# Performance work log

Measured on AMD Instinct MI355X. Metric: run time of the kernel, lower is better.

Reference implementation:

```python
import jax, jax.numpy as jnp
import numpy as np

B, C, H, W = 4, 256, 64, 64
R, KH, KW = 4, 3, 3
K = KH * KW  # 9 kernel taps


def _conv2d(x, w, b):
    # plain 3x3 conv, stride 1, pad 1, NCHW
    y = jax.lax.conv_general_dilated(x, w, (1, 1), ((1, 1), (1, 1)),
                                     dimension_numbers=('NCHW', 'OIHW', 'NCHW'))
    return y + b[None, :, None, None]


def _bilinear_sample(x, py, px):
    # x: [B,C,H,W]; py,px: [B,K,H,W] float coords; zero padding outside the image.
    B_, C_, H_, W_ = x.shape
    xf = x.reshape(B_, C_, H_ * W_)
    y0 = jnp.floor(py)
    x0 = jnp.floor(px)
    wy = py - y0
    wx = px - x0
    y0i = y0.astype(jnp.int32)
    x0i = x0.astype(jnp.int32)

    def corner(yi, xi, wgt):
        valid = (yi >= 0) & (yi < H_) & (xi >= 0) & (xi < W_)
        idx = (jnp.clip(yi, 0, H_ - 1) * W_ + jnp.clip(xi, 0, W_ - 1)).reshape(B_, -1)
        vals = jax.vmap(lambda xb, ib: jnp.take(xb, ib, axis=1))(xf, idx)  # [B,C,K*H*W]
        vals = vals.reshape(B_, C_, K, H_, W_)
        w_ = (wgt * valid).astype(x.dtype)[:, None]  # [B,1,K,H,W]
        return vals * w_

    out = corner(y0i, x0i, (1 - wy) * (1 - wx))
    out = out + corner(y0i, x0i + 1, (1 - wy) * wx)
    out = out + corner(y0i + 1, x0i, wy * (1 - wx))
    out = out + corner(y0i + 1, x0i + 1, wy * wx)
    return out  # [B,C,K,H,W]


def _deform_conv(x, offset, weight):
    # DCNv1: offset [B, 2K, H, W], interleaved (dy, dx) per kernel tap.
    B_, C_, H_, W_ = x.shape
    off = offset.reshape(B_, K, 2, H_, W_)
    ky, kx = jnp.meshgrid(jnp.arange(KH), jnp.arange(KW), indexing='ij')
    base_y = (ky.reshape(K) - (KH - 1) // 2).astype(x.dtype)
    base_x = (kx.reshape(K) - (KW - 1) // 2).astype(x.dtype)
    py = (jnp.arange(H_, dtype=x.dtype)[None, None, :, None]
          + base_y[None, :, None, None] + off[:, :, 0])
    px = (jnp.arange(W_, dtype=x.dtype)[None, None, None, :]
          + base_x[None, :, None, None] + off[:, :, 1])
    sampled = _bilinear_sample(x, py, px)  # [B,C,K,H,W]
    wr = weight.reshape(weight.shape[0], C_, K)
    return jnp.einsum('bckhw,ock->bohw', sampled, wr)


def setup_inputs() -> dict:
    key = jax.random.key(0)
    k1, k2, k3 = jax.random.split(key, 3)
    x = jax.random.normal(k1, (B, C, H, W), jnp.float32)
    off_w = jax.random.normal(k2, (R, 2 * K, C, KH, KW), jnp.float32) * 0.01
    off_b = jnp.zeros((R, 2 * K), jnp.float32)
    w = jax.random.normal(k3, (R, C, C, KH, KW), jnp.float32) * (1.0 / np.sqrt(C * K))
    return {"x": x, "off_w": off_w, "off_b": off_b, "w": w}


def reference(x, off_w, off_b, w):
    for r in range(R):  # fixed small layer count
        offset = _conv2d(x, off_w[r], off_b[r])
        x = jax.nn.relu(_deform_conv(x, offset, w[r]))
    return x
```

## Files before the change

### kernel.cpp

```cpp
#include <hip/hip_runtime.h>


#define HW 4096

typedef __attribute__((ext_vector_type(8))) __bf16 bf16x8;
typedef __attribute__((ext_vector_type(4))) float f32x4;
typedef __attribute__((ext_vector_type(8))) unsigned short u16x8;

__device__ inline unsigned int f2bf_bits(float f) {
  unsigned int u = __float_as_uint(f);
  return (u + 0x7fffu + ((u >> 16) & 1u)) >> 16;
}
__device__ inline float bf_hi_f(unsigned short h) {
  return __uint_as_float(((unsigned int)h) << 16);
}

__device__ inline void wg_barrier_lds() {
  asm volatile("s_waitcnt lgkmcnt(0)" ::: "memory");
  __builtin_amdgcn_s_barrier();
  __builtin_amdgcn_sched_barrier(0);
}

__global__ __launch_bounds__(256) void wpack_kernel(
    const float* __restrict__ w, unsigned short* __restrict__ wph) {
  const int f = blockIdx.x * 256 + threadIdx.x;
  const int j  = f & 7;
  const int l  = (f >> 3) & 63;
  const int nt = (f >> 9) & 15;
  const int q  = (f >> 13) % 72;
  const int r  = f / 589824;
  const int n  = nt * 16 + (l & 15);
  const int kk = q * 32 + ((l >> 4) << 3) + j;
  const int c  = kk & 255, k = kk >> 8;
  wph[f] = (unsigned short)f2bf_bits(w[((r * 256 + n) * 256 + c) * 9 + k]);
}

__global__ __launch_bounds__(256) void offwpack_kernel(
    const float* __restrict__ offw, unsigned short* __restrict__ owph) {
  const int f = blockIdx.x * 256 + threadIdx.x;
  const int j  = f & 7;
  const int l  = (f >> 3) & 63;
  const int nt = (f >> 9) & 1;
  const int q  = (f >> 10) % 72;
  const int r  = f / 73728;
  const int n  = nt * 16 + (l & 15);
  const int kk = q * 32 + ((l >> 4) << 3) + j;
  const int c  = kk & 255, k = kk >> 8;
  const float v = (n < 18) ? offw[((r * 18 + n) * 256 + c) * 9 + k] : 0.f;
  owph[f] = (unsigned short)f2bf_bits(v);
}

__global__ __launch_bounds__(256) void xpose_kernel(
    const float* __restrict__ x, unsigned short* __restrict__ xh) {
  const int p0 = blockIdx.x * 64;
  const int c0 = blockIdx.y * 64;
  const int b  = blockIdx.z;
  __shared__ float sT[64][65];
  const int t = threadIdx.x;
  const int pj = t & 63, ci0 = (t >> 6) * 16;
  const float* __restrict__ xb = x + ((size_t)(b * 256 + c0)) * HW + p0;
#pragma unroll
  for (int u = 0; u < 16; ++u)
    sT[ci0 + u][pj] = xb[(size_t)(ci0 + u) * HW + pj];
  __syncthreads();
  const int pr = t >> 2, cs = (t & 3) * 16;
  u16x8 va, vb;
#pragma unroll
  for (int u = 0; u < 8; ++u) va[u] = (unsigned short)f2bf_bits(sT[cs + u][pr]);
#pragma unroll
  for (int u = 0; u < 8; ++u) vb[u] = (unsigned short)f2bf_bits(sT[cs + 8 + u][pr]);
  const size_t o = ((size_t)b * HW + p0 + pr) * 256 + c0 + cs;
  *(u16x8*)(xh + o) = va;
  *(u16x8*)(xh + o + 8) = vb;
}

__global__ __launch_bounds__(512) void offconv_mfma(
    const unsigned short* __restrict__ xh,
    const unsigned short* __restrict__ owh,
    const float* __restrict__ bias, float* __restrict__ offs) {
  const int gid = blockIdx.x;
  const int b = (gid & 7) >> 1;
  const int idx = ((gid >> 3) << 1) | (gid & 1);
  const int h = idx >> 1, w0 = (idx & 1) << 5;
  const int t = threadIdx.x, lane = t & 63, wv = t >> 6;
  const int frow = lane & 15, fgrp = lane >> 4;
  const int mt = wv & 1, nt = (wv >> 1) & 1, kv = wv >> 2;
  const int m = w0 + mt * 16 + frow;

  f32x4 acc = {0.f, 0.f, 0.f, 0.f};
  const u16x8 z8 = {};
  const size_t xb = (size_t)b * HW;

  for (int k = 0; k < 9; ++k) {
    const int ky = k / 3 - 1, kx = k % 3 - 1;
    if ((unsigned)(h + ky) < 64u) {
      const bool vpx = (unsigned)(m + kx) < 64u;
      const int cpx = (m + kx) < 0 ? 0 : ((m + kx) > 63 ? 63 : (m + kx));
      const size_t abase = (xb + (size_t)((h + ky) * 64 + cpx)) * 256 + fgrp * 8;
#pragma unroll
      for (int j = 0; j < 4; ++j) {
        const int cc = kv * 4 + j;
        const int q = k * 8 + cc;
        u16x8 ahr = *(const u16x8*)(xh + abase + cc * 32);
        if (!vpx) ahr = z8;
        const u16x8 bhr = ((const u16x8*)owh)[(q * 2 + nt) * 64 + lane];
        const bf16x8 ah = __builtin_bit_cast(bf16x8, ahr);
        const bf16x8 bh = __builtin_bit_cast(bf16x8, bhr);
        acc = __builtin_amdgcn_mfma_f32_16x16x32_bf16(ah, bh, acc, 0, 0, 0);
      }
    }
  }

  __shared__ f32x4 red[2][2][64];
  if (kv == 1) red[mt][nt][lane] = acc;
  __syncthreads();
  if (kv == 0) {
    const f32x4 o = red[mt][nt][lane];
    acc[0] += o[0]; acc[1] += o[1]; acc[2] += o[2]; acc[3] += o[3];
    const int oc = nt * 16 + frow;
    if (oc < 18) {
      const float bv = bias[oc];
      const int wbase = w0 + mt * 16 + fgrp * 4;
      float* __restrict__ op =
          offs + (size_t)(b * 18 + oc) * HW + h * 64 + wbase;
#pragma unroll
      for (int r = 0; r < 4; ++r) op[r] = acc[r] + bv;
    }
  }
}

__global__ __launch_bounds__(512, 4) void deform_mfma(
    const unsigned short* __restrict__ xh,
    const float* __restrict__ offs,
    const unsigned short* __restrict__ wph,
    unsigned short* __restrict__ yth,
    float* __restrict__ outf) {
  const int gid = blockIdx.x;
  const int b = (gid & 7) >> 1;
  const int idx = ((gid >> 3) << 1) | (gid & 1);
  const int h = idx >> 1, w0 = (idx & 1) << 5;
  const int t = threadIdx.x, lane = t & 63, wv = t >> 6;
  const int frow = lane & 15, quad = lane >> 4;
  const int sm = t >> 4, cg = t & 15;

  __shared__ __align__(16) unsigned char smem[18432];
  float* s_cw = (float*)smem;
  int*   s_ci = (int*)(smem + 4608);
  unsigned char* sAb = smem + 9216;

  for (int i = t; i < 288; i += 512) {
    const int k = i >> 5, m = i & 31;
    const int ky = k / 3 - 1, kx = k % 3 - 1;
    const int mw = w0 + m;
    const int pos = h * 64 + mw;
    const float dy = offs[(b * 18 + 2 * k) * HW + pos];
    const float dx = offs[(b * 18 + 2 * k + 1) * HW + pos];
    const float py = (float)(h + ky) + dy;
    const float px = (float)(mw + kx) + dx;
    const float y0f = floorf(py), x0f = floorf(px);
    const float wy = py - y0f, wx = px - x0f;
    const int y0 = (int)y0f, x0 = (int)x0f;
#pragma unroll
    for (int j = 0; j < 4; ++j) {
      const int yi = y0 + (j >> 1), xi = x0 + (j & 1);
      const bool v = (yi >= 0) && (yi < 64) && (xi >= 0) && (xi < 64);
      const float wgt = ((j >> 1) ? wy : 1.f - wy) * ((j & 1) ? wx : 1.f - wx);
      s_cw[(k * 4 + j) * 32 + m] = v ? wgt : 0.f;
      const int yc = yi < 0 ? 0 : (yi > 63 ? 63 : yi);
      const int xc = xi < 0 ? 0 : (xi > 63 ? 63 : xi);
      s_ci[(k * 4 + j) * 32 + m] = yc * 64 + xc;
    }
  }
  __syncthreads();

  f32x4 acc[2][2];
#pragma unroll
  for (int mt = 0; mt < 2; ++mt)
#pragma unroll
    for (int nt = 0; nt < 2; ++nt) acc[mt][nt] = (f32x4){0.f, 0.f, 0.f, 0.f};

  const char* __restrict__ xbc = (const char*)(xh + (size_t)b * HW * 256);
  const u16x8* __restrict__ wp = (const u16x8*)wph;
  const int bfo = wv * 2;

  const int gs = ((sm & 3) << 1) | ((sm >> 2) & 1);
  const int wbA = sm * 128 + ((((cg >> 2) ^ gs)) << 4) + (cg & 3) * 4;
  const int wbL = wbA ^ 64;
  const int gr = ((frow & 3) << 1) | ((frow >> 2) & 1);
  const int rb0 = frow * 128 + ((quad ^ gr) << 4);
  const int rb1 = rb0 + 2048;

  unsigned int G0[4], G1[4];
  u16x8 B0[2], B1[2];
  float cwrC[4], cwrN[4];
  int cibC[4], cibN[4];
#pragma unroll
  for (int j = 0; j < 4; ++j) {
    cwrC[j] = s_cw[j * 32 + sm];
    cibC[j] = s_ci[j * 32 + sm] * 512;
  }
#pragma unroll
  for (int j = 0; j < 4; ++j)
    G0[j] = *(const unsigned int*)(xbc + cibC[j] + cg * 4);
#pragma unroll
  for (int j = 0; j < 4; ++j)
    G1[j] = *(const unsigned int*)(xbc + cibC[j] + 64 + cg * 4);
#pragma unroll
  for (int i = 0; i < 2; ++i) B0[i] = wp[(bfo + i) * 64 + lane];
#pragma unroll
  for (int i = 0; i < 2; ++i) B1[i] = wp[(16 + bfo + i) * 64 + lane];

#define COMBINE_STORE(Gx, buf)                                              \
  {                                                                         \
    float s0 = cwrC[0] * __uint_as_float(Gx[0] << 16);                      \
    float s1 = cwrC[0] * __uint_as_float(Gx[0] & 0xffff0000u);              \
    s0 = fmaf(cwrC[1], __uint_as_float(Gx[1] << 16), s0);                   \
    s1 = fmaf(cwrC[1], __uint_as_float(Gx[1] & 0xffff0000u), s1);           \
    s0 = fmaf(cwrC[2], __uint_as_float(Gx[2] << 16), s0);                   \
    s1 = fmaf(cwrC[2], __uint_as_float(Gx[2] & 0xffff0000u), s1);           \
    s0 = fmaf(cwrC[3], __uint_as_float(Gx[3] << 16), s0);                   \
    s1 = fmaf(cwrC[3], __uint_as_float(Gx[3] & 0xffff0000u), s1);           \
    const unsigned int h0 = f2bf_bits(s0), h1 = f2bf_bits(s1);              \
    const unsigned int l0 = f2bf_bits(s0 - __uint_as_float(h0 << 16));      \
    const unsigned int l1 = f2bf_bits(s1 - __uint_as_float(h1 << 16));      \
    *(unsigned int*)(sAb + (buf) * 4096 + wbA) = h0 | (h1 << 16);           \
    *(unsigned int*)(sAb + (buf) * 4096 + wbL) = l0 | (l1 << 16);           \
  }

#define MFMA_BODY(buf, Bx)                                                  \
  {                                                                         \
    bf16x8 ah[2], al[2];                                                    \
    ah[0] = __builtin_bit_cast(                                             \
        bf16x8, *(const u16x8*)(sAb + (buf) * 4096 + rb0));                 \
    al[0] = __builtin_bit_cast(                                             \
        bf16x8, *(const u16x8*)(sAb + (buf) * 4096 + (rb0 ^ 64)));          \
    ah[1] = __builtin_bit_cast(                                             \
        bf16x8, *(const u16x8*)(sAb + (buf) * 4096 + rb1));                 \
    al[1] = __builtin_bit_cast(                                             \
        bf16x8, *(const u16x8*)(sAb + (buf) * 4096 + (rb1 ^ 64)));          \
    __builtin_amdgcn_s_setprio(1);                                          \
    _Pragma("unroll") for (int nt = 0; nt < 2; ++nt) {                      \
      const bf16x8 bv = __builtin_bit_cast(bf16x8, Bx[nt]);                 \
      _Pragma("unroll") for (int mt = 0; mt < 2; ++mt) {                    \
        acc[mt][nt] = __builtin_amdgcn_mfma_f32_16x16x32_bf16(              \
            ah[mt], bv, acc[mt][nt], 0, 0, 0);                              \
        acc[mt][nt] = __builtin_amdgcn_mfma_f32_16x16x32_bf16(              \
            al[mt], bv, acc[mt][nt], 0, 0, 0);                              \
      }                                                                     \
    }                                                                       \
    __builtin_amdgcn_s_setprio(0);                                          \
  }

  for (int k9 = 0; k9 < 9; ++k9) {
    const int cbase = k9 * 8;
#pragma unroll
    for (int j4 = 0; j4 < 4; ++j4) {
      COMBINE_STORE(G0, 0)
      wg_barrier_lds();
      if (k9 < 8 || j4 < 3) {
        if (j4 == 3) {
#pragma unroll
          for (int j = 0; j < 4; ++j) {
            cwrN[j] = s_cw[((k9 + 1) * 4 + j) * 32 + sm];
            cibN[j] = s_ci[((k9 + 1) * 4 + j) * 32 + sm] * 512;
          }
#pragma unroll
          for (int j = 0; j < 4; ++j)
            G0[j] = *(const unsigned int*)(xbc + cibN[j] + cg * 4);
        } else {
          const int c0b = (2 * j4 + 2) * 64 + cg * 4;
#pragma unroll
          for (int j = 0; j < 4; ++j)
            G0[j] = *(const unsigned int*)(xbc + cibC[j] + c0b);
        }
      }
      MFMA_BODY(0, B0)
      if (k9 < 8 || j4 < 3) {
        const int c2 = cbase + 2 * j4 + 2;
#pragma unroll
        for (int i = 0; i < 2; ++i)
          B0[i] = wp[(c2 * 16 + bfo + i) * 64 + lane];
      }
      COMBINE_STORE(G1, 1)
      wg_barrier_lds();
      if (k9 < 8 || j4 < 3) {
        if (j4 == 3) {
#pragma unroll
          for (int j = 0; j < 4; ++j)
            G1[j] = *(const unsigned int*)(xbc + cibN[j] + 64 + cg * 4);
        } else {
          const int c1b = (2 * j4 + 3) * 64 + cg * 4;
#pragma unroll
          for (int j = 0; j < 4; ++j)
            G1[j] = *(const unsigned int*)(xbc + cibC[j] + c1b);
        }
      }
      MFMA_BODY(1, B1)
      if (k9 < 8 || j4 < 3) {
        const int c3 = cbase + 2 * j4 + 3;
#pragma unroll
        for (int i = 0; i < 2; ++i)
          B1[i] = wp[(c3 * 16 + bfo + i) * 64 + lane];
      }
      if (j4 == 3 && k9 < 8) {
#pragma unroll
        for (int j = 0; j < 4; ++j) { cwrC[j] = cwrN[j]; cibC[j] = cibN[j]; }
      }
    }
  }
#undef COMBINE_STORE
#undef MFMA_BODY

  if (outf) {
#pragma unroll
    for (int mt = 0; mt < 2; ++mt)
#pragma unroll
      for (int nt = 0; nt < 2; ++nt) {
        const int n = wv * 32 + nt * 16 + frow;
        const int pos = h * 64 + w0 + mt * 16 + quad * 4;
        float4 vv;
        vv.x = fmaxf(acc[mt][nt][0], 0.f);
        vv.y = fmaxf(acc[mt][nt][1], 0.f);
        vv.z = fmaxf(acc[mt][nt][2], 0.f);
        vv.w = fmaxf(acc[mt][nt][3], 0.f);
        *(float4*)&outf[(size_t)(b * 256 + n) * HW + pos] = vv;
      }
  } else {
    __syncthreads();
    unsigned short* sW = (unsigned short*)smem + wv * (32 * 36);
#pragma unroll
    for (int mt = 0; mt < 2; ++mt)
#pragma unroll
      for (int nt = 0; nt < 2; ++nt)
#pragma unroll
        for (int r = 0; r < 4; ++r)
          sW[(mt * 16 + quad * 4 + r) * 36 + nt * 16 + frow] =
              (unsigned short)f2bf_bits(fmaxf(acc[mt][nt][r], 0.f));
    __syncthreads();
    const int lm = lane & 31, cg2 = lane >> 5;
    const int pos = h * 64 + w0 + lm;
    unsigned short* __restrict__ yp =
        yth + ((size_t)b * HW + pos) * 256 + wv * 32 + cg2 * 16;
#pragma unroll
    for (int g = 0; g < 2; ++g)
      *(u16x8*)(yp + g * 8) = *(const u16x8*)&sW[lm * 36 + cg2 * 16 + g * 8];
  }
}

extern "C" void kernel_launch(void* const* d_in, const int* in_sizes, int n_in,
                              void* d_out, int out_size, void* d_ws, size_t ws_size,
                              hipStream_t stream) {
  const float* x0   = (const float*)d_in[0];
  const float* offw = (const float*)d_in[1];
  const float* offb = (const float*)d_in[2];
  const float* w    = (const float*)d_in[3];
  float* out = (float*)d_out;
  float* ws  = (float*)d_ws;

  float* offs = ws;
  unsigned short* wph  = (unsigned short*)(ws + 294912);
  unsigned short* owph = wph + 2359296;
  unsigned short* xTA  = owph + 294912;
  unsigned short* xTB  = xTA + 4194304;

  wpack_kernel<<<9216, 256, 0, stream>>>(w, wph);
  offwpack_kernel<<<1152, 256, 0, stream>>>(offw, owph);
  xpose_kernel<<<dim3(64, 4, 4), 256, 0, stream>>>(x0, xTA);

  unsigned short* pin = xTA;
  unsigned short* pout = xTB;
  for (int r = 0; r < 4; ++r) {
    offconv_mfma<<<512, 512, 0, stream>>>(pin, owph + r * 73728,
                                          offb + r * 18, offs);
    deform_mfma<<<512, 512, 0, stream>>>(pin, offs,
                                         wph + (size_t)r * 589824,
                                         (r < 3) ? pout : nullptr,
                                         (r < 3) ? nullptr : out);
    unsigned short* tmp = pin; pin = pout; pout = tmp;
  }
}
```

Before: 357.6 us.

## Halve deform barriers with 4-slot LDS ring and software-pipeline offset conv loads

The deform kernel now combines and stores two channel-group A tiles per step into a ping-pong pair of LDS buffer sets (4 slots, larger shared allocation), so each step needs one workgroup barrier instead of two. The offset-conv kernel is rewritten as an explicitly double-buffered load/MFMA sequence with clamped addresses, letting global loads for the next tap overlap the current MFMAs. The bf16 hi/lo split now uses native __bf16 casts instead of manual rounding. These add register pressure and LDS use, which may reduce occupancy.

```diff
diff --git a/kernel.cpp b/kernel.cpp
--- a/kernel.cpp
+++ b/kernel.cpp
@@ -90,26 +90,46 @@
   f32x4 acc = {0.f, 0.f, 0.f, 0.f};
   const u16x8 z8 = {};
   const size_t xb = (size_t)b * HW;
-
-  for (int k = 0; k < 9; ++k) {
-    const int ky = k / 3 - 1, kx = k % 3 - 1;
-    if ((unsigned)(h + ky) < 64u) {
-      const bool vpx = (unsigned)(m + kx) < 64u;
-      const int cpx = (m + kx) < 0 ? 0 : ((m + kx) > 63 ? 63 : (m + kx));
-      const size_t abase = (xb + (size_t)((h + ky) * 64 + cpx)) * 256 + fgrp * 8;
-#pragma unroll
-      for (int j = 0; j < 4; ++j) {
-        const int cc = kv * 4 + j;
-        const int q = k * 8 + cc;
-        u16x8 ahr = *(const u16x8*)(xh + abase + cc * 32);
-        if (!vpx) ahr = z8;
-        const u16x8 bhr = ((const u16x8*)owh)[(q * 2 + nt) * 64 + lane];
-        const bf16x8 ah = __builtin_bit_cast(bf16x8, ahr);
-        const bf16x8 bh = __builtin_bit_cast(bf16x8, bhr);
-        acc = __builtin_amdgcn_mfma_f32_16x16x32_bf16(ah, bh, acc, 0, 0, 0);
-      }
-    }
-  }
+  const u16x8* __restrict__ owp = (const u16x8*)owh;
+
+#define OLOAD(k, A, Bv)                                                     \
+  {                                                                         \
+    const int ky = (k) / 3 - 1, kx = (k) % 3 - 1;                           \
+    const int hy = h + ky;                                                  \
+    const int hyc = hy < 0 ? 0 : (hy > 63 ? 63 : hy);                       \
+    const int mx = m + kx;                                                  \
+    const bool v = ((unsigned)hy < 64u) && ((unsigned)mx < 64u);            \
+    const int cpx = mx < 0 ? 0 : (mx > 63 ? 63 : mx);                       \
+    const size_t abase =                                                    \
+        (xb + (size_t)(hyc * 64 + cpx)) * 256 + fgrp * 8 + kv * 128;        \
+    _Pragma("unroll") for (int j = 0; j < 4; ++j) {                         \
+      A[j] = *(const u16x8*)(xh + abase + j * 32);                          \
+      if (!v) A[j] = z8;                                                    \
+    }                                                                       \
+    _Pragma("unroll") for (int j = 0; j < 4; ++j)                           \
+      Bv[j] = owp[((((k) * 8 + kv * 4 + j) * 2) + nt) * 64 + lane];         \
+  }
+
+#define OMFMA(A, Bv)                                                        \
+  _Pragma("unroll") for (int j = 0; j < 4; ++j)                             \
+    acc = __builtin_amdgcn_mfma_f32_16x16x32_bf16(                          \
+        __builtin_bit_cast(bf16x8, A[j]), __builtin_bit_cast(bf16x8, Bv[j]),\
+        acc, 0, 0, 0);
+
+  u16x8 A0[4], Bv0[4], A1[4], Bv1[4];
+  OLOAD(0, A0, Bv0)
+  OLOAD(1, A1, Bv1)
+  OMFMA(A0, Bv0) OLOAD(2, A0, Bv0)
+  OMFMA(A1, Bv1) OLOAD(3, A1, Bv1)
+  OMFMA(A0, Bv0) OLOAD(4, A0, Bv0)
+  OMFMA(A1, Bv1) OLOAD(5, A1, Bv1)
+  OMFMA(A0, Bv0) OLOAD(6, A0, Bv0)
+  OMFMA(A1, Bv1) OLOAD(7, A1, Bv1)
+  OMFMA(A0, Bv0) OLOAD(8, A0, Bv0)
+  OMFMA(A1, Bv1)
+  OMFMA(A0, Bv0)
+#undef OLOAD
+#undef OMFMA
 
   __shared__ f32x4 red[2][2][64];
   if (kv == 1) red[mt][nt][lane] = acc;
@@ -143,7 +163,7 @@
   const int frow = lane & 15, quad = lane >> 4;
   const int sm = t >> 4, cg = t & 15;
 
-  __shared__ __align__(16) unsigned char smem[18432];
+  __shared__ __align__(16) unsigned char smem[25600];
   float* s_cw = (float*)smem;
   int*   s_ci = (int*)(smem + 4608);
   unsigned char* sAb = smem + 9216;
@@ -210,7 +230,7 @@
 #pragma unroll
   for (int i = 0; i < 2; ++i) B1[i] = wp[(16 + bfo + i) * 64 + lane];
 
-#define COMBINE_STORE(Gx, buf)                                              \
+#define COMBINE_STORE(Gx, BB)                                               \
   {                                                                         \
     float s0 = cwrC[0] * __uint_as_float(Gx[0] << 16);                      \
     float s1 = cwrC[0] * __uint_as_float(Gx[0] & 0xffff0000u);              \
@@ -220,24 +240,29 @@
     s1 = fmaf(cwrC[2], __uint_as_float(Gx[2] & 0xffff0000u), s1);           \
     s0 = fmaf(cwrC[3], __uint_as_float(Gx[3] << 16), s0);                   \
     s1 = fmaf(cwrC[3], __uint_as_float(Gx[3] & 0xffff0000u), s1);           \
-    const unsigned int h0 = f2bf_bits(s0), h1 = f2bf_bits(s1);              \
-    const unsigned int l0 = f2bf_bits(s0 - __uint_as_float(h0 << 16));      \
-    const unsigned int l1 = f2bf_bits(s1 - __uint_as_float(h1 << 16));      \
-    *(unsigned int*)(sAb + (buf) * 4096 + wbA) = h0 | (h1 << 16);           \
-    *(unsigned int*)(sAb + (buf) * 4096 + wbL) = l0 | (l1 << 16);           \
-  }
-
-#define MFMA_BODY(buf, Bx)                                                  \
+    const __bf16 hb0 = (__bf16)s0, hb1 = (__bf16)s1;                        \
+    const unsigned int hv =                                                 \
+        (unsigned int)__builtin_bit_cast(unsigned short, hb0) |             \
+        ((unsigned int)__builtin_bit_cast(unsigned short, hb1) << 16);      \
+    const float d0 = s0 - __uint_as_float(hv << 16);                        \
+    const float d1 = s1 - __uint_as_float(hv & 0xffff0000u);                \
+    const __bf16 lb0 = (__bf16)d0, lb1 = (__bf16)d1;                        \
+    const unsigned int lv =                                                 \
+        (unsigned int)__builtin_bit_cast(unsigned short, lb0) |             \
+        ((unsigned int)__builtin_bit_cast(unsigned short, lb1) << 16);      \
+    *(unsigned int*)(sAb + (BB) + wbA) = hv;                                \
+    *(unsigned int*)(sAb + (BB) + wbL) = lv;                                \
+  }
+
+#define MFMA_BODY(BB, Bx)                                                   \
   {                                                                         \
     bf16x8 ah[2], al[2];                                                    \
-    ah[0] = __builtin_bit_cast(                                             \
-        bf16x8, *(const u16x8*)(sAb + (buf) * 4096 + rb0));                 \
-    al[0] = __builtin_bit_cast(                                             \
-        bf16x8, *(const u16x8*)(sAb + (buf) * 4096 + (rb0 ^ 64)));          \
-    ah[1] = __builtin_bit_cast(                                             \
-        bf16x8, *(const u16x8*)(sAb + (buf) * 4096 + rb1));                 \
-    al[1] = __builtin_bit_cast(                                             \
-        bf16x8, *(const u16x8*)(sAb + (buf) * 4096 + (rb1 ^ 64)));          \
+    ah[0] = __builtin_bit_cast(bf16x8, *(const u16x8*)(sAb + (BB) + rb0));  \
+    al[0] = __builtin_bit_cast(bf16x8,                                      \
+                               *(const u16x8*)(sAb + (BB) + (rb0 ^ 64)));   \
+    ah[1] = __builtin_bit_cast(bf16x8, *(const u16x8*)(sAb + (BB) + rb1));  \
+    al[1] = __builtin_bit_cast(bf16x8,                                      \
+                               *(const u16x8*)(sAb + (BB) + (rb1 ^ 64)));   \
     __builtin_amdgcn_s_setprio(1);                                          \
     _Pragma("unroll") for (int nt = 0; nt < 2; ++nt) {                      \
       const bf16x8 bv = __builtin_bit_cast(bf16x8, Bx[nt]);                 \
@@ -252,13 +277,15 @@
   }
 
   for (int k9 = 0; k9 < 9; ++k9) {
-    const int cbase = k9 * 8;
-#pragma unroll
-    for (int j4 = 0; j4 < 4; ++j4) {
-      COMBINE_STORE(G0, 0)
+#pragma unroll
+    for (int sp = 0; sp < 4; ++sp) {
+      const int PB = (sp & 1) * 8192;
+      COMBINE_STORE(G0, PB)
+      COMBINE_STORE(G1, PB + 4096)
       wg_barrier_lds();
-      if (k9 < 8 || j4 < 3) {
-        if (j4 == 3) {
+      const bool more = (k9 < 8) || (sp < 3);
+      if (more) {
+        if (sp == 3) {
 #pragma unroll
           for (int j = 0; j < 4; ++j) {
             cwrN[j] = s_cw[((k9 + 1) * 4 + j) * 32 + sm];
@@ -267,42 +294,34 @@
 #pragma unroll
           for (int j = 0; j < 4; ++j)
             G0[j] = *(const unsigned int*)(xbc + cibN[j] + cg * 4);
-        } else {
-          const int c0b = (2 * j4 + 2) * 64 + cg * 4;
-#pragma unroll
-          for (int j = 0; j < 4; ++j)
-            G0[j] = *(const unsigned int*)(xbc + cibC[j] + c0b);
-        }
-      }
-      MFMA_BODY(0, B0)
-      if (k9 < 8 || j4 < 3) {
-        const int c2 = cbase + 2 * j4 + 2;
-#pragma unroll
-        for (int i = 0; i < 2; ++i)
-          B0[i] = wp[(c2 * 16 + bfo + i) * 64 + lane];
-      }
-      COMBINE_STORE(G1, 1)
-      wg_barrier_lds();
-      if (k9 < 8 || j4 < 3) {
-        if (j4 == 3) {
 #pragma unroll
           for (int j = 0; j < 4; ++j)
             G1[j] = *(const unsigned int*)(xbc + cibN[j] + 64 + cg * 4);
         } else {
-          const int c1b = (2 * j4 + 3) * 64 + cg * 4;
+          const int c0b = ((2 * sp + 2) & 7) * 64 + cg * 4;
 #pragma unroll
           for (int j = 0; j < 4; ++j)
-            G1[j] = *(const unsigned int*)(xbc + cibC[j] + c1b);
+            G0[j] = *(const unsigned int*)(xbc + cibC[j] + c0b);
+#pragma unroll
+          for (int j = 0; j < 4; ++j)
+            G1[j] = *(const unsigned int*)(xbc + cibC[j] + c0b + 64);
         }
       }
-      MFMA_BODY(1, B1)
-      if (k9 < 8 || j4 < 3) {
-        const int c3 = cbase + 2 * j4 + 3;
+      MFMA_BODY(PB, B0)
+      if (more) {
+        const int cn0 = k9 * 8 + 2 * sp + 2;
 #pragma unroll
         for (int i = 0; i < 2; ++i)
-          B1[i] = wp[(c3 * 16 + bfo + i) * 64 + lane];
+          B0[i] = wp[(cn0 * 16 + bfo + i) * 64 + lane];
       }
-      if (j4 == 3 && k9 < 8) {
+      MFMA_BODY(PB + 4096, B1)
+      if (more) {
+        const int cn1 = k9 * 8 + 2 * sp + 3;
+#pragma unroll
+        for (int i = 0; i < 2; ++i)
+          B1[i] = wp[(cn1 * 16 + bfo + i) * 64 + lane];
+      }
+      if (sp == 3 && k9 < 8) {
 #pragma unroll
         for (int j = 0; j < 4; ++j) { cwrC[j] = cwrN[j]; cibC[j] = cibN[j]; }
       }
```

New measurement: 346.8 us. -3.0%, faster.
